# Optimization experiments

Hardware: AMD Instinct MI355X
Metric: run time of the kernel (lower is better)

The kernel has to match this reference:

```python
import jax, jax.numpy as jnp
import numpy as np

B, S, H, I, E_ROUTED, TOP_K = 8, 2048, 1024, 2048, 8, 2


def _expert(x, Wg, Wu, Wd):
    # SwiGLU expert: down(silu(gate(x)) * up(x)); Linear weights stored [out, in]
    return (jax.nn.silu(x @ Wg.T) * (x @ Wu.T)) @ Wd.T


def setup_inputs() -> dict:
    key = jax.random.key(0)
    ks = jax.random.split(key, 9)
    s = 0.02  # init scale
    return {
        "x": jax.random.normal(ks[0], (B, S, H), dtype=jnp.float32),
        # shared expert (num_shared = 1)
        "Wg_s": jax.random.normal(ks[1], (I, H), dtype=jnp.float32) * s,
        "Wu_s": jax.random.normal(ks[2], (I, H), dtype=jnp.float32) * s,
        "Wd_s": jax.random.normal(ks[3], (H, I), dtype=jnp.float32) * s,
        # routed experts, stacked [E, ...]
        "Wg": jax.random.normal(ks[4], (E_ROUTED, I, H), dtype=jnp.float32) * s,
        "Wu": jax.random.normal(ks[5], (E_ROUTED, I, H), dtype=jnp.float32) * s,
        "Wd": jax.random.normal(ks[6], (E_ROUTED, H, I), dtype=jnp.float32) * s,
        # router
        "Wr": jax.random.normal(ks[7], (E_ROUTED, H), dtype=jnp.float32) * s,
        "rb": jnp.zeros((E_ROUTED,), dtype=jnp.float32),
    }


def reference(x, Wg_s, Wu_s, Wd_s, Wg, Wu, Wd, Wr, rb):
    # shared experts (num_shared = 1, so mean == the single expert output)
    shared = _expert(x, Wg_s, Wu_s, Wd_s)  # [B,S,H]

    # sigmoid top-k routing
    logits = jnp.einsum('bsh,eh->bse', x, Wr) + rb        # [B,S,E]
    probs = jax.nn.sigmoid(logits)
    scores, idx = jax.lax.top_k(probs, TOP_K)             # [B,S,K]

    # dense combine weights: cw[b,s,e] = sum_k scores[b,s,k] * 1[idx[b,s,k]==e]
    cw = (jax.nn.one_hot(idx, E_ROUTED, dtype=x.dtype) * scores[..., None]).sum(-2)  # [B,S,E]

    out = shared
    for e in range(E_ROUTED):  # small fixed expert count
        out = out + cw[..., e:e + 1] * _expert(x, Wg[e], Wu[e], Wd[e])
    return out
```

## Files before the change

kernel.cpp:

```cpp
#include <hip/hip_runtime.h>

#define T_TOK 16384
#define HDIM  1024
#define IDIM  2048
#define NEXP  8
#define CNT_STRIDE 32
#define TOK_PER_BLK 32
#define MAX_RTILES 264

typedef __attribute__((ext_vector_type(8))) short bf16x8;
typedef __attribute__((ext_vector_type(4))) float f32x4;
typedef unsigned short u16;
typedef unsigned int u32;

typedef __attribute__((address_space(1))) const unsigned int gas_u32;
typedef __attribute__((address_space(3))) unsigned int las_u32;

__device__ __forceinline__ void gl16(const void* g, void* l) {
  __builtin_amdgcn_global_load_lds((gas_u32*)g, (las_u32*)l, 16, 0, 0);
}

__device__ __forceinline__ u16 f2bf(float f) {
  union { float f; u32 i; } v; v.f = f;
  u32 r = v.i + 0x7FFF + ((v.i >> 16) & 1);
  return (u16)(r >> 16);
}
__device__ __forceinline__ u32 pack2(float a, float b) {
  return (u32)f2bf(a) | ((u32)f2bf(b) << 16);
}

__global__ __launch_bounds__(256) void cvt_kernel(
    const float* __restrict__ s, u16* __restrict__ d, int n)
{
  int i = (blockIdx.x * 256 + threadIdx.x) * 4;
  if (i < n) {
    f32x4 v = *(const f32x4*)(s + i);
    uint2 o; o.x = pack2(v[0], v[1]); o.y = pack2(v[2], v[3]);
    *(uint2*)(d + i) = o;
  }
}

__global__ void init_counts(int* counts) {
  counts[threadIdx.x] = 0;
}

__global__ __launch_bounds__(256) void router_kernel(
    const float* __restrict__ x, const float* __restrict__ Wr,
    const float* __restrict__ rb, float* __restrict__ cw,
    int* __restrict__ counts, int* __restrict__ lists)
{
  __shared__ __align__(16) float sWr[NEXP * HDIM];
  __shared__ int pickE[2 * TOK_PER_BLK];
  __shared__ int pickT[2 * TOK_PER_BLK];

  const int tid = threadIdx.x;
  const int lane = tid & 63;
  const int wv = tid >> 6;

  for (int i = tid; i < NEXP * HDIM / 4; i += 256)
    ((f32x4*)sWr)[i] = ((const f32x4*)Wr)[i];

  float rbl[NEXP];
  #pragma unroll
  for (int e = 0; e < NEXP; ++e) rbl[e] = rb[e];

  __syncthreads();

  const int t_base = blockIdx.x * TOK_PER_BLK + wv * (TOK_PER_BLK / 4);
  for (int j = 0; j < TOK_PER_BLK / 4; ++j) {
    const int t = t_base + j;
    const float* xrow = x + (size_t)t * HDIM;
    f32x4 xv[4];
    #pragma unroll
    for (int c = 0; c < 4; ++c) xv[c] = *(const f32x4*)(xrow + c * 256 + lane * 4);

    double acc[NEXP];
    #pragma unroll
    for (int e = 0; e < NEXP; ++e) {
      const float* wr = sWr + e * HDIM;
      double a = 0.0;
      #pragma unroll
      for (int c = 0; c < 4; ++c) {
        f32x4 w4 = *(const f32x4*)(wr + c * 256 + lane * 4);
        a += (double)xv[c][0] * (double)w4[0];
        a += (double)xv[c][1] * (double)w4[1];
        a += (double)xv[c][2] * (double)w4[2];
        a += (double)xv[c][3] * (double)w4[3];
      }
      acc[e] = a;
    }
    #pragma unroll
    for (int e = 0; e < NEXP; ++e) {
      double a = acc[e];
      a += __shfl_xor(a, 1, 64);
      a += __shfl_xor(a, 2, 64);
      a += __shfl_xor(a, 4, 64);
      acc[e] = a;
    }
    double s0 = (lane & 1) ? acc[1] : acc[0];
    double s1 = (lane & 1) ? acc[3] : acc[2];
    double s2 = (lane & 1) ? acc[5] : acc[4];
    double s3 = (lane & 1) ? acc[7] : acc[6];
    double u0 = (lane & 2) ? s1 : s0;
    double u1 = (lane & 2) ? s3 : s2;
    double v  = (lane & 4) ? u1 : u0;
    v += __shfl_xor(v, 8, 64);
    v += __shfl_xor(v, 16, 64);
    v += __shfl_xor(v, 32, 64);
    double l[NEXP];
    #pragma unroll
    for (int e = 0; e < NEXP; ++e) l[e] = __shfl(v, e, 64) + (double)rbl[e];

    if (lane == 0) {
      int i1 = 0;
      #pragma unroll
      for (int e = 1; e < NEXP; ++e) if (l[e] > l[i1]) i1 = e;
      int i2 = -1;
      #pragma unroll
      for (int e = 0; e < NEXP; ++e) {
        if (e == i1) continue;
        if (i2 < 0 || l[e] > l[i2]) i2 = e;
      }
      float p1 = (float)(1.0 / (1.0 + exp(-l[i1])));
      float p2 = (float)(1.0 / (1.0 + exp(-l[i2])));
      cw[(size_t)t * NEXP + i1] = p1;
      cw[(size_t)t * NEXP + i2] = p2;
      int slot = (wv * (TOK_PER_BLK / 4) + j) * 2;
      pickE[slot] = i1; pickE[slot + 1] = i2;
      pickT[slot] = t;  pickT[slot + 1] = t;
    }
  }
  __syncthreads();

  const int myE = pickE[lane];
  const int myT = pickT[lane];
  #pragma unroll
  for (int ei = 0; ei < 2; ++ei) {
    int e = wv + ei * 4;
    unsigned long long b = __ballot(myE == e);
    int cnt = __popcll(b);
    int base = 0;
    if (lane == 0) base = atomicAdd(&counts[e * CNT_STRIDE], cnt);
    base = __shfl(base, 0, 64);
    if (myE == e)
      lists[(size_t)e * T_TOK + base + __popcll(b & ((1ull << lane) - 1))] = myT;
  }
}

__global__ void build_tiles(const int* __restrict__ counts,
                            int* __restrict__ td_e, int* __restrict__ td_r0,
                            int* __restrict__ ntiles)
{
  if (threadIdx.x == 0) {
    int n = 0;
    for (int e = 0; e < NEXP; ++e) {
      int c = counts[e * CNT_STRIDE];
      for (int r = 0; r < c; r += 128) { td_e[n] = e; td_r0[n] = r; ++n; }
    }
    *ntiles = n;
  }
}

template<int SRC>
__global__ __launch_bounds__(256, 2) void moe_gateup_k(
    const u16* __restrict__ xb, const float* __restrict__ xf,
    const u16* __restrict__ Wg_b, const u16* __restrict__ Wu_b,
    const float* __restrict__ Wg_f, const float* __restrict__ Wu_f,
    const int* __restrict__ list, const int* __restrict__ count_ptr,
    u16* __restrict__ hbuf, int c0)
{
  __shared__ __align__(16) u16 sA[128 * 32];
  __shared__ __align__(16) u16 sG[128 * 32];
  __shared__ __align__(16) u16 sU[128 * 32];

  const int cnt = count_ptr ? *count_ptr : T_TOK;
  const int remain = cnt - c0;
  const int m0 = blockIdx.y * 128;
  if (m0 >= remain) return;
  const int n0 = blockIdx.x * 128;

  const int tid = threadIdx.x, lane = tid & 63, w = tid >> 6;
  const int wm = w & 1, wn = w >> 1;
  const int quad = lane >> 4, l15 = lane & 15;

  const int srow0 = w * 32 + (lane >> 2);
  const int srow1 = srow0 + 16;
  const int kch = (lane & 3) * 8;
  const int ar = lane >> 3, ac = lane & 7;

  const u16 *pa0 = nullptr, *pa1 = nullptr, *pg0 = nullptr, *pg1 = nullptr,
            *pu0 = nullptr, *pu1 = nullptr;
  const float *fa[4], *fg[4], *fu[4];
  int frow[4];

  if (SRC == 0) {
    int gi0 = c0 + m0 + srow0, gi1 = c0 + m0 + srow1;
    int tok0 = (gi0 < cnt) ? (list ? list[gi0] : gi0) : 0;
    int tok1 = (gi1 < cnt) ? (list ? list[gi1] : gi1) : 0;
    pa0 = xb + (size_t)tok0 * HDIM + kch;
    pa1 = xb + (size_t)tok1 * HDIM + kch;
    pg0 = Wg_b + (size_t)(n0 + srow0) * HDIM + kch;
    pg1 = Wg_b + (size_t)(n0 + srow1) * HDIM + kch;
    pu0 = Wu_b + (size_t)(n0 + srow0) * HDIM + kch;
    pu1 = Wu_b + (size_t)(n0 + srow1) * HDIM + kch;
  } else {
    #pragma unroll
    for (int p = 0; p < 4; ++p) {
      int row = w * 32 + p * 8 + ar;
      frow[p] = row;
      int gi = c0 + m0 + row;
      int tok = (gi < cnt) ? (list ? list[gi] : gi) : 0;
      fa[p] = xf + (size_t)tok * HDIM + ac * 4;
      fg[p] = Wg_f + (size_t)(n0 + row) * HDIM + ac * 4;
      fu[p] = Wu_f + (size_t)(n0 + row) * HDIM + ac * 4;
    }
  }

  const u16* fA = sA + (wm * 64 + l15) * 32 + quad * 8;
  const u16* fG = sG + (wn * 64 + l15) * 32 + quad * 8;
  const u16* fU = sU + (wn * 64 + l15) * 32 + quad * 8;

  f32x4 accG[4][4] = {};
  f32x4 accU[4][4] = {};

  for (int kt = 0; kt < HDIM / 32; ++kt) {
    if (SRC == 0) {
      gl16(pa0 + kt * 32, sA + w * 1024);
      gl16(pa1 + kt * 32, sA + w * 1024 + 512);
      gl16(pg0 + kt * 32, sG + w * 1024);
      gl16(pg1 + kt * 32, sG + w * 1024 + 512);
      gl16(pu0 + kt * 32, sU + w * 1024);
      gl16(pu1 + kt * 32, sU + w * 1024 + 512);
    } else {
      #pragma unroll
      for (int p = 0; p < 4; ++p) {
        f32x4 va = *(const f32x4*)(fa[p] + kt * 32);
        f32x4 vg = *(const f32x4*)(fg[p] + kt * 32);
        f32x4 vu = *(const f32x4*)(fu[p] + kt * 32);
        uint2 oa; oa.x = pack2(va[0], va[1]); oa.y = pack2(va[2], va[3]);
        uint2 og; og.x = pack2(vg[0], vg[1]); og.y = pack2(vg[2], vg[3]);
        uint2 ou; ou.x = pack2(vu[0], vu[1]); ou.y = pack2(vu[2], vu[3]);
        *(uint2*)(sA + frow[p] * 32 + ac * 4) = oa;
        *(uint2*)(sG + frow[p] * 32 + ac * 4) = og;
        *(uint2*)(sU + frow[p] * 32 + ac * 4) = ou;
      }
    }
    __syncthreads();
    bf16x8 a[4];
    #pragma unroll
    for (int mt = 0; mt < 4; ++mt) a[mt] = *(const bf16x8*)(fA + mt * 16 * 32);
    #pragma unroll
    for (int nt = 0; nt < 4; ++nt) {
      bf16x8 bg = *(const bf16x8*)(fG + nt * 16 * 32);
      bf16x8 bu = *(const bf16x8*)(fU + nt * 16 * 32);
      #pragma unroll
      for (int mt = 0; mt < 4; ++mt) {
        accG[mt][nt] = __builtin_amdgcn_mfma_f32_16x16x32_bf16(a[mt], bg, accG[mt][nt], 0, 0, 0);
        accU[mt][nt] = __builtin_amdgcn_mfma_f32_16x16x32_bf16(a[mt], bu, accU[mt][nt], 0, 0, 0);
      }
    }
    __syncthreads();
  }

  #pragma unroll
  for (int mt = 0; mt < 4; ++mt) {
    #pragma unroll
    for (int i = 0; i < 4; ++i) {
      int row = m0 + wm * 64 + mt * 16 + quad * 4 + i;
      if (row < remain) {
        u16* orow = hbuf + (size_t)row * IDIM + n0 + wn * 64 + l15;
        #pragma unroll
        for (int nt = 0; nt < 4; ++nt) {
          float g = accG[mt][nt][i], u = accU[mt][nt][i];
          float h = (g / (1.f + __expf(-g))) * u;
          orow[nt * 16] = f2bf(h);
        }
      }
    }
  }
}

template<int SRC>
__global__ __launch_bounds__(256, 2) void moe_down_k(
    const u16* __restrict__ hbuf,
    const u16* __restrict__ Wd_b, const float* __restrict__ Wd_f,
    const int* __restrict__ list, const int* __restrict__ count_ptr,
    const float* __restrict__ cw, int expert, float* __restrict__ out, int c0)
{
  __shared__ __align__(16) u16 sA[128 * 32];
  __shared__ __align__(16) u16 sB[128 * 32];

  const int cnt = count_ptr ? *count_ptr : T_TOK;
  const int remain = cnt - c0;
  const int m0 = blockIdx.y * 128;
  if (m0 >= remain) return;
  const int n0 = blockIdx.x * 128;

  const int tid = threadIdx.x, lane = tid & 63, w = tid >> 6;
  const int wm = w & 1, wn = w >> 1;
  const int quad = lane >> 4, l15 = lane & 15;

  const int srow0 = w * 32 + (lane >> 2);
  const int srow1 = srow0 + 16;
  const int kch = (lane & 3) * 8;
  const int ar = lane >> 3, ac = lane & 7;

  const u16* pa0 = hbuf + (size_t)(m0 + srow0) * IDIM + kch;
  const u16* pa1 = hbuf + (size_t)(m0 + srow1) * IDIM + kch;
  const u16 *pb0 = nullptr, *pb1 = nullptr;
  const float* fb[4];
  int frow[4];
  if (SRC == 0) {
    pb0 = Wd_b + (size_t)(n0 + srow0) * IDIM + kch;
    pb1 = Wd_b + (size_t)(n0 + srow1) * IDIM + kch;
  } else {
    #pragma unroll
    for (int p = 0; p < 4; ++p) {
      int row = w * 32 + p * 8 + ar;
      frow[p] = row;
      fb[p] = Wd_f + (size_t)(n0 + row) * IDIM + ac * 4;
    }
  }

  const u16* fA = sA + (wm * 64 + l15) * 32 + quad * 8;
  const u16* fB = sB + (wn * 64 + l15) * 32 + quad * 8;

  f32x4 acc[4][4] = {};

  for (int kt = 0; kt < IDIM / 32; ++kt) {
    gl16(pa0 + kt * 32, sA + w * 1024);
    gl16(pa1 + kt * 32, sA + w * 1024 + 512);
    if (SRC == 0) {
      gl16(pb0 + kt * 32, sB + w * 1024);
      gl16(pb1 + kt * 32, sB + w * 1024 + 512);
    } else {
      #pragma unroll
      for (int p = 0; p < 4; ++p) {
        f32x4 v = *(const f32x4*)(fb[p] + kt * 32);
        uint2 o; o.x = pack2(v[0], v[1]); o.y = pack2(v[2], v[3]);
        *(uint2*)(sB + frow[p] * 32 + ac * 4) = o;
      }
    }
    __syncthreads();
    bf16x8 a[4];
    #pragma unroll
    for (int mt = 0; mt < 4; ++mt) a[mt] = *(const bf16x8*)(fA + mt * 16 * 32);
    #pragma unroll
    for (int nt = 0; nt < 4; ++nt) {
      bf16x8 b = *(const bf16x8*)(fB + nt * 16 * 32);
      #pragma unroll
      for (int mt = 0; mt < 4; ++mt)
        acc[mt][nt] = __builtin_amdgcn_mfma_f32_16x16x32_bf16(a[mt], b, acc[mt][nt], 0, 0, 0);
    }
    __syncthreads();
  }

  #pragma unroll
  for (int mt = 0; mt < 4; ++mt) {
    #pragma unroll
    for (int i = 0; i < 4; ++i) {
      int rl = m0 + wm * 64 + mt * 16 + quad * 4 + i;
      if (rl < remain) {
        int token = list ? list[c0 + rl] : (c0 + rl);
        float s = (expert >= 0) ? cw[(size_t)token * NEXP + expert] : 1.f;
        float* orow = out + (size_t)token * HDIM + n0 + wn * 64 + l15;
        #pragma unroll
        for (int nt = 0; nt < 4; ++nt) {
          float v = s * acc[mt][nt][i];
          if (expert >= 0) v += orow[nt * 16];
          orow[nt * 16] = v;
        }
      }
    }
  }
}

__global__ __launch_bounds__(256, 2) void moe_gateup_fused(
    const u16* __restrict__ xb,
    const u16* __restrict__ Wg_b, const u16* __restrict__ Wu_b,
    const int* __restrict__ lists, const int* __restrict__ counts,
    const int* __restrict__ td_e, const int* __restrict__ td_r0,
    const int* __restrict__ ntiles,
    u16* __restrict__ hbuf, int t0)
{
  __shared__ __align__(16) u16 sA[128 * 32];
  __shared__ __align__(16) u16 sG[128 * 32];
  __shared__ __align__(16) u16 sU[128 * 32];

  const int ty = t0 + blockIdx.y;
  if (ty >= *ntiles) return;
  const int e = td_e[ty];
  const int r0 = td_r0[ty];
  const int cnt = counts[e * CNT_STRIDE];
  const int* list = lists + (size_t)e * T_TOK;
  const size_t WSH = (size_t)IDIM * HDIM;
  const u16* Wg_e = Wg_b + (size_t)e * WSH;
  const u16* Wu_e = Wu_b + (size_t)e * WSH;
  const int n0 = blockIdx.x * 128;

  const int tid = threadIdx.x, lane = tid & 63, w = tid >> 6;
  const int wm = w & 1, wn = w >> 1;
  const int quad = lane >> 4, l15 = lane & 15;

  const int srow0 = w * 32 + (lane >> 2);
  const int srow1 = srow0 + 16;
  const int kch = (lane & 3) * 8;

  int gi0 = r0 + srow0, gi1 = r0 + srow1;
  int tok0 = (gi0 < cnt) ? list[gi0] : 0;
  int tok1 = (gi1 < cnt) ? list[gi1] : 0;
  const u16* pa0 = xb + (size_t)tok0 * HDIM + kch;
  const u16* pa1 = xb + (size_t)tok1 * HDIM + kch;
  const u16* pg0 = Wg_e + (size_t)(n0 + srow0) * HDIM + kch;
  const u16* pg1 = Wg_e + (size_t)(n0 + srow1) * HDIM + kch;
  const u16* pu0 = Wu_e + (size_t)(n0 + srow0) * HDIM + kch;
  const u16* pu1 = Wu_e + (size_t)(n0 + srow1) * HDIM + kch;

  const u16* fA = sA + (wm * 64 + l15) * 32 + quad * 8;
  const u16* fG = sG + (wn * 64 + l15) * 32 + quad * 8;
  const u16* fU = sU + (wn * 64 + l15) * 32 + quad * 8;

  f32x4 accG[4][4] = {};
  f32x4 accU[4][4] = {};

  for (int kt = 0; kt < HDIM / 32; ++kt) {
    gl16(pa0 + kt * 32, sA + w * 1024);
    gl16(pa1 + kt * 32, sA + w * 1024 + 512);
    gl16(pg0 + kt * 32, sG + w * 1024);
    gl16(pg1 + kt * 32, sG + w * 1024 + 512);
    gl16(pu0 + kt * 32, sU + w * 1024);
    gl16(pu1 + kt * 32, sU + w * 1024 + 512);
    __syncthreads();
    bf16x8 a[4];
    #pragma unroll
    for (int mt = 0; mt < 4; ++mt) a[mt] = *(const bf16x8*)(fA + mt * 16 * 32);
    #pragma unroll
    for (int nt = 0; nt < 4; ++nt) {
      bf16x8 bg = *(const bf16x8*)(fG + nt * 16 * 32);
      bf16x8 bu = *(const bf16x8*)(fU + nt * 16 * 32);
      #pragma unroll
      for (int mt = 0; mt < 4; ++mt) {
        accG[mt][nt] = __builtin_amdgcn_mfma_f32_16x16x32_bf16(a[mt], bg, accG[mt][nt], 0, 0, 0);
        accU[mt][nt] = __builtin_amdgcn_mfma_f32_16x16x32_bf16(a[mt], bu, accU[mt][nt], 0, 0, 0);
      }
    }
    __syncthreads();
  }

  #pragma unroll
  for (int mt = 0; mt < 4; ++mt) {
    #pragma unroll
    for (int i = 0; i < 4; ++i) {
      int rl = wm * 64 + mt * 16 + quad * 4 + i;
      u16* orow = hbuf + (size_t)(blockIdx.y * 128 + rl) * IDIM + n0 + wn * 64 + l15;
      #pragma unroll
      for (int nt = 0; nt < 4; ++nt) {
        float g = accG[mt][nt][i], u = accU[mt][nt][i];
        float h = (g / (1.f + __expf(-g))) * u;
        orow[nt * 16] = f2bf(h);
      }
    }
  }
}

__global__ __launch_bounds__(256, 2) void moe_down_fused(
    const u16* __restrict__ hbuf, const u16* __restrict__ Wd_b,
    const int* __restrict__ lists, const int* __restrict__ counts,
    const int* __restrict__ td_e, const int* __restrict__ td_r0,
    const int* __restrict__ ntiles,
    const float* __restrict__ cw, float* __restrict__ out, int t0)
{
  __shared__ __align__(16) u16 sA[128 * 32];
  __shared__ __align__(16) u16 sB[128 * 32];

  const int ty = t0 + blockIdx.y;
  if (ty >= *ntiles) return;
  const int e = td_e[ty];
  const int r0 = td_r0[ty];
  const int cnt = counts[e * CNT_STRIDE];
  const int* list = lists + (size_t)e * T_TOK;
  const size_t WSH = (size_t)IDIM * HDIM;
  const u16* Wd_e = Wd_b + (size_t)e * WSH;
  const int n0 = blockIdx.x * 128;

  const int tid = threadIdx.x, lane = tid & 63, w = tid >> 6;
  const int wm = w & 1, wn = w >> 1;
  const int quad = lane >> 4, l15 = lane & 15;

  const int srow0 = w * 32 + (lane >> 2);
  const int srow1 = srow0 + 16;
  const int kch = (lane & 3) * 8;

  const u16* pa0 = hbuf + (size_t)(blockIdx.y * 128 + srow0) * IDIM + kch;
  const u16* pa1 = hbuf + (size_t)(blockIdx.y * 128 + srow1) * IDIM + kch;
  const u16* pb0 = Wd_e + (size_t)(n0 + srow0) * IDIM + kch;
  const u16* pb1 = Wd_e + (size_t)(n0 + srow1) * IDIM + kch;

  const u16* fA = sA + (wm * 64 + l15) * 32 + quad * 8;
  const u16* fB = sB + (wn * 64 + l15) * 32 + quad * 8;

  f32x4 acc[4][4] = {};

  for (int kt = 0; kt < IDIM / 32; ++kt) {
    gl16(pa0 + kt * 32, sA + w * 1024);
    gl16(pa1 + kt * 32, sA + w * 1024 + 512);
    gl16(pb0 + kt * 32, sB + w * 1024);
    gl16(pb1 + kt * 32, sB + w * 1024 + 512);
    __syncthreads();
    bf16x8 a[4];
    #pragma unroll
    for (int mt = 0; mt < 4; ++mt) a[mt] = *(const bf16x8*)(fA + mt * 16 * 32);
    #pragma unroll
    for (int nt = 0; nt < 4; ++nt) {
      bf16x8 b = *(const bf16x8*)(fB + nt * 16 * 32);
      #pragma unroll
      for (int mt = 0; mt < 4; ++mt)
        acc[mt][nt] = __builtin_amdgcn_mfma_f32_16x16x32_bf16(a[mt], b, acc[mt][nt], 0, 0, 0);
    }
    __syncthreads();
  }

  #pragma unroll
  for (int mt = 0; mt < 4; ++mt) {
    #pragma unroll
    for (int i = 0; i < 4; ++i) {
      int rl = wm * 64 + mt * 16 + quad * 4 + i;
      if (r0 + rl < cnt) {
        int token = list[r0 + rl];
        float s = cw[(size_t)token * NEXP + e];
        float* orow = out + (size_t)token * HDIM + n0 + wn * 64 + l15;
        #pragma unroll
        for (int nt = 0; nt < 4; ++nt)
          atomicAdd(&orow[nt * 16], s * acc[mt][nt][i]);
      }
    }
  }
}

extern "C" void kernel_launch(void* const* d_in, const int* in_sizes, int n_in,
                              void* d_out, int out_size, void* d_ws, size_t ws_size,
                              hipStream_t stream) {
  (void)in_sizes; (void)n_in; (void)out_size;
  const float* x    = (const float*)d_in[0];
  const float* Wg_s = (const float*)d_in[1];
  const float* Wu_s = (const float*)d_in[2];
  const float* Wd_s = (const float*)d_in[3];
  const float* Wg   = (const float*)d_in[4];
  const float* Wu   = (const float*)d_in[5];
  const float* Wd   = (const float*)d_in[6];
  const float* Wr   = (const float*)d_in[7];
  const float* rb   = (const float*)d_in[8];
  float* out = (float*)d_out;

  char* ws = (char*)d_ws;
  size_t off = 1024;
  int* counts = (int*)ws;
  int* lists = (int*)(ws + off);  off += (size_t)NEXP * T_TOK * 4;
  float* cw = (float*)(ws + off); off += (size_t)T_TOK * NEXP * 4;
  int* td = (int*)(ws + off);     off += 2304;
  int* td_e = td;
  int* td_r0 = td + MAX_RTILES;
  int* ntiles = td + 2 * MAX_RTILES;

  const size_t WSH = (size_t)IDIM * HDIM;
  const size_t xc_elems = (size_t)T_TOK * HDIM;
  const size_t wc_elems = 3 * WSH + 3 * NEXP * WSH;
  const size_t fast_need = off + (xc_elems + wc_elems) * 2 + (size_t)2048 * IDIM * 2;
  const bool fast = ws_size >= fast_need;

  u16* xc = (u16*)(ws + off);
  u16* wgs_c = xc + (fast ? xc_elems : 0);
  u16* wus_c = wgs_c + WSH;
  u16* wds_c = wus_c + WSH;
  u16* wg_c = wds_c + WSH;
  u16* wu_c = wg_c + NEXP * WSH;
  u16* wd_c = wu_c + NEXP * WSH;

  size_t hoff = off + (fast ? (xc_elems + wc_elems) * 2 : 0);
  u16* hbuf = (u16*)(ws + hoff);

  size_t avail = (ws_size > hoff) ? (ws_size - hoff) : 0;
  long long capll = (long long)(avail / ((size_t)IDIM * 2));
  int cap = (capll > T_TOK) ? T_TOK : (int)capll;
  cap &= ~127;
  if (cap < 128) cap = 128;
  int nchunks = (T_TOK + cap - 1) / cap;

  init_counts<<<1, NEXP * CNT_STRIDE, 0, stream>>>(counts);
  if (fast) {
    auto cv = [&](const float* s, u16* d, size_t n) {
      int blocks = (int)((n / 4 + 255) / 256);
      cvt_kernel<<<blocks, 256, 0, stream>>>(s, d, (int)n);
    };
    cv(x, xc, xc_elems);
    cv(Wg_s, wgs_c, WSH); cv(Wu_s, wus_c, WSH); cv(Wd_s, wds_c, WSH);
    cv(Wg, wg_c, NEXP * WSH); cv(Wu, wu_c, NEXP * WSH); cv(Wd, wd_c, NEXP * WSH);
  }
  router_kernel<<<T_TOK / TOK_PER_BLK, 256, 0, stream>>>(x, Wr, rb, cw, counts, lists);

  dim3 blk(256);
  dim3 gA(IDIM / 128, cap / 128);
  dim3 gB(HDIM / 128, cap / 128);

  for (int c = 0; c < nchunks; ++c) {
    int c0 = c * cap;
    if (fast) {
      moe_gateup_k<0><<<gA, blk, 0, stream>>>(xc, nullptr, wgs_c, wus_c, nullptr, nullptr,
                                              nullptr, nullptr, hbuf, c0);
      moe_down_k<0><<<gB, blk, 0, stream>>>(hbuf, wds_c, nullptr, nullptr, nullptr,
                                            cw, -1, out, c0);
    } else {
      moe_gateup_k<1><<<gA, blk, 0, stream>>>(nullptr, x, nullptr, nullptr, Wg_s, Wu_s,
                                              nullptr, nullptr, hbuf, c0);
      moe_down_k<1><<<gB, blk, 0, stream>>>(hbuf, nullptr, Wd_s, nullptr, nullptr,
                                            cw, -1, out, c0);
    }
  }

  if (fast) {
    build_tiles<<<1, 64, 0, stream>>>(counts, td_e, td_r0, ntiles);
    int tpc = cap / 128;
    for (int t0 = 0; t0 < MAX_RTILES; t0 += tpc) {
      int ytiles = (MAX_RTILES - t0 < tpc) ? (MAX_RTILES - t0) : tpc;
      dim3 gAf(IDIM / 128, ytiles);
      dim3 gBf(HDIM / 128, ytiles);
      moe_gateup_fused<<<gAf, blk, 0, stream>>>(xc, wg_c, wu_c, lists, counts,
                                                td_e, td_r0, ntiles, hbuf, t0);
      moe_down_fused<<<gBf, blk, 0, stream>>>(hbuf, wd_c, lists, counts,
                                              td_e, td_r0, ntiles, cw, out, t0);
    }
  } else {
    for (int e = 0; e < NEXP; ++e) {
      const int* lst = lists + (size_t)e * T_TOK;
      const int* cptr = counts + (size_t)e * CNT_STRIDE;
      for (int c = 0; c < nchunks; ++c) {
        int c0 = c * cap;
        moe_gateup_k<1><<<gA, blk, 0, stream>>>(nullptr, x, nullptr, nullptr,
                                                Wg + (size_t)e * WSH, Wu + (size_t)e * WSH,
                                                lst, cptr, hbuf, c0);
        moe_down_k<1><<<gB, blk, 0, stream>>>(hbuf, nullptr, Wd + (size_t)e * WSH,
                                              lst, cptr, cw, e, out, c0);
      }
    }
  }
}
```

Baseline: 1.272 ms.

## Merge shared expert into routed tile list with BK=64 swizzled tiles and 256-wide down

Folds the shared expert into the same tile descriptor list as the routed experts (expert id -1), so one pair of grouped GEMM launches covers all work. Output is zeroed first and every contribution is accumulated with atomics. The kernels now use a K-tile of 64 with an XOR-swizzled LDS layout to avoid bank conflicts and halve the barrier count. The down projection uses a 128x256 tile to get more reuse per loaded A tile. The costs are more atomic traffic on the shared-expert output, a separate zeroing pass, and larger LDS use that may limit occupancy.

```diff
diff --git a/kernel.cpp b/kernel.cpp
--- a/kernel.cpp
+++ b/kernel.cpp
@@ -6,7 +6,7 @@
 #define NEXP  8
 #define CNT_STRIDE 32
 #define TOK_PER_BLK 32
-#define MAX_RTILES 264
+#define MAX_TILES 400
 
 typedef __attribute__((ext_vector_type(8))) short bf16x8;
 typedef __attribute__((ext_vector_type(4))) float f32x4;
@@ -42,6 +42,12 @@
 
 __global__ void init_counts(int* counts) {
   counts[threadIdx.x] = 0;
+}
+
+__global__ __launch_bounds__(256) void zero_kernel(float* __restrict__ p, int n4) {
+  f32x4 z = {0.f, 0.f, 0.f, 0.f};
+  for (int i = blockIdx.x * 256 + threadIdx.x; i < n4; i += gridDim.x * 256)
+    ((f32x4*)p)[i] = z;
 }
 
 __global__ __launch_bounds__(256) void router_kernel(
@@ -153,6 +159,7 @@
 {
   if (threadIdx.x == 0) {
     int n = 0;
+    for (int r = 0; r < T_TOK; r += 128) { td_e[n] = -1; td_r0[n] = r; ++n; }
     for (int e = 0; e < NEXP; ++e) {
       int c = counts[e * CNT_STRIDE];
       for (int r = 0; r < c; r += 128) { td_e[n] = e; td_r0[n] = r; ++n; }
@@ -161,10 +168,201 @@
   }
 }
 
-template<int SRC>
+
+__global__ __launch_bounds__(256, 2) void gateup128f(
+    const u16* __restrict__ xb,
+    const u16* __restrict__ Wg_sh, const u16* __restrict__ Wu_sh,
+    const u16* __restrict__ Wg_rt, const u16* __restrict__ Wu_rt,
+    const int* __restrict__ lists, const int* __restrict__ counts,
+    const int* __restrict__ td_e, const int* __restrict__ td_r0,
+    const int* __restrict__ ntiles,
+    u16* __restrict__ hbuf, int t0)
+{
+  __shared__ __align__(16) u16 sA[128 * 64];
+  __shared__ __align__(16) u16 sG[128 * 64];
+  __shared__ __align__(16) u16 sU[128 * 64];
+
+  const int ty = t0 + blockIdx.y;
+  if (ty >= *ntiles) return;
+  const int e = td_e[ty];
+  const int r0 = td_r0[ty];
+  const size_t WSH = (size_t)IDIM * HDIM;
+  int cnt; const int* list; const u16 *Wg_e, *Wu_e;
+  if (e < 0) { cnt = T_TOK; list = nullptr; Wg_e = Wg_sh; Wu_e = Wu_sh; }
+  else {
+    cnt = counts[e * CNT_STRIDE]; list = lists + (size_t)e * T_TOK;
+    Wg_e = Wg_rt + (size_t)e * WSH; Wu_e = Wu_rt + (size_t)e * WSH;
+  }
+  const int n0 = blockIdx.x * 128;
+
+  const int tid = threadIdx.x, lane = tid & 63, w = tid >> 6;
+  const int wm = w & 1, wn = w >> 1;
+  const int quad = lane >> 4, l15 = lane & 15, l7 = lane & 7;
+  const int drow = lane >> 3;
+  const int sslot = (lane & 7) ^ drow;
+
+  const u16 *pa[4], *pg[4], *pu[4];
+  u16 *dA[4], *dG[4], *dU[4];
+  #pragma unroll
+  for (int c = 0; c < 4; ++c) {
+    int row = w * 32 + c * 8 + drow;
+    int gi = r0 + row;
+    int tok = list ? ((gi < cnt) ? list[gi] : 0) : gi;
+    pa[c] = xb + (size_t)tok * HDIM + sslot * 8;
+    pg[c] = Wg_e + (size_t)(n0 + row) * HDIM + sslot * 8;
+    pu[c] = Wu_e + (size_t)(n0 + row) * HDIM + sslot * 8;
+    dA[c] = sA + (w * 32 + c * 8) * 64;
+    dG[c] = sG + (w * 32 + c * 8) * 64;
+    dU[c] = sU + (w * 32 + c * 8) * 64;
+  }
+
+  const u16* fA = sA + (wm * 64 + l15) * 64;
+  const u16* fG = sG + (wn * 64 + l15) * 64;
+  const u16* fU = sU + (wn * 64 + l15) * 64;
+
+  f32x4 accG[4][4] = {};
+  f32x4 accU[4][4] = {};
+
+  for (int kt = 0; kt < HDIM / 64; ++kt) {
+    #pragma unroll
+    for (int c = 0; c < 4; ++c) {
+      gl16(pa[c] + kt * 64, dA[c]);
+      gl16(pg[c] + kt * 64, dG[c]);
+      gl16(pu[c] + kt * 64, dU[c]);
+    }
+    __syncthreads();
+    #pragma unroll
+    for (int ks = 0; ks < 2; ++ks) {
+      const int sw = ((ks * 4 + quad) ^ l7) * 8;
+      bf16x8 a[4], bg[4], bu[4];
+      #pragma unroll
+      for (int mt = 0; mt < 4; ++mt) a[mt] = *(const bf16x8*)(fA + mt * 1024 + sw);
+      #pragma unroll
+      for (int nt = 0; nt < 4; ++nt) {
+        bg[nt] = *(const bf16x8*)(fG + nt * 1024 + sw);
+        bu[nt] = *(const bf16x8*)(fU + nt * 1024 + sw);
+      }
+      #pragma unroll
+      for (int nt = 0; nt < 4; ++nt) {
+        #pragma unroll
+        for (int mt = 0; mt < 4; ++mt) {
+          accG[mt][nt] = __builtin_amdgcn_mfma_f32_16x16x32_bf16(a[mt], bg[nt], accG[mt][nt], 0, 0, 0);
+          accU[mt][nt] = __builtin_amdgcn_mfma_f32_16x16x32_bf16(a[mt], bu[nt], accU[mt][nt], 0, 0, 0);
+        }
+      }
+    }
+    __syncthreads();
+  }
+
+  #pragma unroll
+  for (int mt = 0; mt < 4; ++mt) {
+    #pragma unroll
+    for (int i = 0; i < 4; ++i) {
+      int rl = wm * 64 + mt * 16 + quad * 4 + i;
+      u16* orow = hbuf + (size_t)(blockIdx.y * 128 + rl) * IDIM + n0 + wn * 64 + l15;
+      #pragma unroll
+      for (int nt = 0; nt < 4; ++nt) {
+        float g = accG[mt][nt][i], u = accU[mt][nt][i];
+        float h = (g / (1.f + __expf(-g))) * u;
+        orow[nt * 16] = f2bf(h);
+      }
+    }
+  }
+}
+
+__global__ __launch_bounds__(256, 2) void down256f(
+    const u16* __restrict__ hbuf,
+    const u16* __restrict__ Wd_sh, const u16* __restrict__ Wd_rt,
+    const int* __restrict__ lists, const int* __restrict__ counts,
+    const int* __restrict__ td_e, const int* __restrict__ td_r0,
+    const int* __restrict__ ntiles,
+    const float* __restrict__ cw, float* __restrict__ out, int t0)
+{
+  __shared__ __align__(16) u16 sA[128 * 64];
+  __shared__ __align__(16) u16 sB[256 * 64];
+
+  const int ty = t0 + blockIdx.y;
+  if (ty >= *ntiles) return;
+  const int e = td_e[ty];
+  const int r0 = td_r0[ty];
+  const size_t WSH = (size_t)IDIM * HDIM;
+  int cnt; const int* list; const u16* Wd_e;
+  if (e < 0) { cnt = T_TOK; list = nullptr; Wd_e = Wd_sh; }
+  else {
+    cnt = counts[e * CNT_STRIDE]; list = lists + (size_t)e * T_TOK;
+    Wd_e = Wd_rt + (size_t)e * WSH;
+  }
+  const int n0 = blockIdx.x * 256;
+
+  const int tid = threadIdx.x, lane = tid & 63, w = tid >> 6;
+  const int wm = w & 1, wn = w >> 1;
+  const int quad = lane >> 4, l15 = lane & 15, l7 = lane & 7;
+  const int drow = lane >> 3;
+  const int sslot = (lane & 7) ^ drow;
+
+  const u16 *pa[4], *pb[8];
+  u16 *dA[4], *dB[8];
+  #pragma unroll
+  for (int c = 0; c < 4; ++c) {
+    int row = w * 32 + c * 8 + drow;
+    pa[c] = hbuf + (size_t)(blockIdx.y * 128 + row) * IDIM + sslot * 8;
+    dA[c] = sA + (w * 32 + c * 8) * 64;
+  }
+  #pragma unroll
+  for (int c = 0; c < 8; ++c) {
+    int row = w * 64 + c * 8 + drow;
+    pb[c] = Wd_e + (size_t)(n0 + row) * IDIM + sslot * 8;
+    dB[c] = sB + (w * 64 + c * 8) * 64;
+  }
+
+  const u16* fA = sA + (wm * 64 + l15) * 64;
+  const u16* fB = sB + (wn * 128 + l15) * 64;
+
+  f32x4 acc[4][8] = {};
+
+  for (int kt = 0; kt < IDIM / 64; ++kt) {
+    #pragma unroll
+    for (int c = 0; c < 4; ++c) gl16(pa[c] + kt * 64, dA[c]);
+    #pragma unroll
+    for (int c = 0; c < 8; ++c) gl16(pb[c] + kt * 64, dB[c]);
+    __syncthreads();
+    #pragma unroll
+    for (int ks = 0; ks < 2; ++ks) {
+      const int sw = ((ks * 4 + quad) ^ l7) * 8;
+      bf16x8 a[4], b[8];
+      #pragma unroll
+      for (int mt = 0; mt < 4; ++mt) a[mt] = *(const bf16x8*)(fA + mt * 1024 + sw);
+      #pragma unroll
+      for (int nt = 0; nt < 8; ++nt) b[nt] = *(const bf16x8*)(fB + nt * 1024 + sw);
+      #pragma unroll
+      for (int nt = 0; nt < 8; ++nt) {
+        #pragma unroll
+        for (int mt = 0; mt < 4; ++mt)
+          acc[mt][nt] = __builtin_amdgcn_mfma_f32_16x16x32_bf16(a[mt], b[nt], acc[mt][nt], 0, 0, 0);
+      }
+    }
+    __syncthreads();
+  }
+
+  #pragma unroll
+  for (int mt = 0; mt < 4; ++mt) {
+    #pragma unroll
+    for (int i = 0; i < 4; ++i) {
+      int rl = wm * 64 + mt * 16 + quad * 4 + i;
+      if (r0 + rl < cnt) {
+        int token = list ? list[r0 + rl] : (r0 + rl);
+        float s = (e >= 0) ? cw[(size_t)token * NEXP + e] : 1.f;
+        float* orow = out + (size_t)token * HDIM + n0 + wn * 128 + l15;
+        #pragma unroll
+        for (int nt = 0; nt < 8; ++nt)
+          atomicAdd(&orow[nt * 16], s * acc[mt][nt][i]);
+      }
+    }
+  }
+}
+
 __global__ __launch_bounds__(256, 2) void moe_gateup_k(
-    const u16* __restrict__ xb, const float* __restrict__ xf,
-    const u16* __restrict__ Wg_b, const u16* __restrict__ Wu_b,
+    const float* __restrict__ xf,
     const float* __restrict__ Wg_f, const float* __restrict__ Wu_f,
     const int* __restrict__ list, const int* __restrict__ count_ptr,
     u16* __restrict__ hbuf, int c0)
@@ -182,38 +380,19 @@
   const int tid = threadIdx.x, lane = tid & 63, w = tid >> 6;
   const int wm = w & 1, wn = w >> 1;
   const int quad = lane >> 4, l15 = lane & 15;
-
-  const int srow0 = w * 32 + (lane >> 2);
-  const int srow1 = srow0 + 16;
-  const int kch = (lane & 3) * 8;
   const int ar = lane >> 3, ac = lane & 7;
 
-  const u16 *pa0 = nullptr, *pa1 = nullptr, *pg0 = nullptr, *pg1 = nullptr,
-            *pu0 = nullptr, *pu1 = nullptr;
   const float *fa[4], *fg[4], *fu[4];
   int frow[4];
-
-  if (SRC == 0) {
-    int gi0 = c0 + m0 + srow0, gi1 = c0 + m0 + srow1;
-    int tok0 = (gi0 < cnt) ? (list ? list[gi0] : gi0) : 0;
-    int tok1 = (gi1 < cnt) ? (list ? list[gi1] : gi1) : 0;
-    pa0 = xb + (size_t)tok0 * HDIM + kch;
-    pa1 = xb + (size_t)tok1 * HDIM + kch;
-    pg0 = Wg_b + (size_t)(n0 + srow0) * HDIM + kch;
-    pg1 = Wg_b + (size_t)(n0 + srow1) * HDIM + kch;
-    pu0 = Wu_b + (size_t)(n0 + srow0) * HDIM + kch;
-    pu1 = Wu_b + (size_t)(n0 + srow1) * HDIM + kch;
-  } else {
-    #pragma unroll
-    for (int p = 0; p < 4; ++p) {
-      int row = w * 32 + p * 8 + ar;
-      frow[p] = row;
-      int gi = c0 + m0 + row;
-      int tok = (gi < cnt) ? (list ? list[gi] : gi) : 0;
-      fa[p] = xf + (size_t)tok * HDIM + ac * 4;
-      fg[p] = Wg_f + (size_t)(n0 + row) * HDIM + ac * 4;
-      fu[p] = Wu_f + (size_t)(n0 + row) * HDIM + ac * 4;
-    }
+  #pragma unroll
+  for (int p = 0; p < 4; ++p) {
+    int row = w * 32 + p * 8 + ar;
+    frow[p] = row;
+    int gi = c0 + m0 + row;
+    int tok = (gi < cnt) ? (list ? list[gi] : gi) : 0;
+    fa[p] = xf + (size_t)tok * HDIM + ac * 4;
+    fg[p] = Wg_f + (size_t)(n0 + row) * HDIM + ac * 4;
+    fu[p] = Wu_f + (size_t)(n0 + row) * HDIM + ac * 4;
   }
 
   const u16* fA = sA + (wm * 64 + l15) * 32 + quad * 8;
@@ -224,26 +403,17 @@
   f32x4 accU[4][4] = {};
 
   for (int kt = 0; kt < HDIM / 32; ++kt) {
-    if (SRC == 0) {
-      gl16(pa0 + kt * 32, sA + w * 1024);
-      gl16(pa1 + kt * 32, sA + w * 1024 + 512);
-      gl16(pg0 + kt * 32, sG + w * 1024);
-      gl16(pg1 + kt * 32, sG + w * 1024 + 512);
-      gl16(pu0 + kt * 32, sU + w * 1024);
-      gl16(pu1 + kt * 32, sU + w * 1024 + 512);
-    } else {
-      #pragma unroll
-      for (int p = 0; p < 4; ++p) {
-        f32x4 va = *(const f32x4*)(fa[p] + kt * 32);
-        f32x4 vg = *(const f32x4*)(fg[p] + kt * 32);
-        f32x4 vu = *(const f32x4*)(fu[p] + kt * 32);
-        uint2 oa; oa.x = pack2(va[0], va[1]); oa.y = pack2(va[2], va[3]);
-        uint2 og; og.x = pack2(vg[0], vg[1]); og.y = pack2(vg[2], vg[3]);
-        uint2 ou; ou.x = pack2(vu[0], vu[1]); ou.y = pack2(vu[2], vu[3]);
-        *(uint2*)(sA + frow[p] * 32 + ac * 4) = oa;
-        *(uint2*)(sG + frow[p] * 32 + ac * 4) = og;
-        *(uint2*)(sU + frow[p] * 32 + ac * 4) = ou;
-      }
+    #pragma unroll
+    for (int p = 0; p < 4; ++p) {
+      f32x4 va = *(const f32x4*)(fa[p] + kt * 32);
+      f32x4 vg = *(const f32x4*)(fg[p] + kt * 32);
+      f32x4 vu = *(const f32x4*)(fu[p] + kt * 32);
+      uint2 oa; oa.x = pack2(va[0], va[1]); oa.y = pack2(va[2], va[3]);
+      uint2 og; og.x = pack2(vg[0], vg[1]); og.y = pack2(vg[2], vg[3]);
+      uint2 ou; ou.x = pack2(vu[0], vu[1]); ou.y = pack2(vu[2], vu[3]);
+      *(uint2*)(sA + frow[p] * 32 + ac * 4) = oa;
+      *(uint2*)(sG + frow[p] * 32 + ac * 4) = og;
+      *(uint2*)(sU + frow[p] * 32 + ac * 4) = ou;
     }
     __syncthreads();
     bf16x8 a[4];
@@ -280,10 +450,8 @@
   }
 }
 
-template<int SRC>
 __global__ __launch_bounds__(256, 2) void moe_down_k(
-    const u16* __restrict__ hbuf,
-    const u16* __restrict__ Wd_b, const float* __restrict__ Wd_f,
+    const u16* __restrict__ hbuf, const float* __restrict__ Wd_f,
     const int* __restrict__ list, const int* __restrict__ count_ptr,
     const float* __restrict__ cw, int expert, float* __restrict__ out, int c0)
 {
@@ -307,19 +475,13 @@
 
   const u16* pa0 = hbuf + (size_t)(m0 + srow0) * IDIM + kch;
   const u16* pa1 = hbuf + (size_t)(m0 + srow1) * IDIM + kch;
-  const u16 *pb0 = nullptr, *pb1 = nullptr;
   const float* fb[4];
   int frow[4];
-  if (SRC == 0) {
-    pb0 = Wd_b + (size_t)(n0 + srow0) * IDIM + kch;
-    pb1 = Wd_b + (size_t)(n0 + srow1) * IDIM + kch;
-  } else {
-    #pragma unroll
-    for (int p = 0; p < 4; ++p) {
-      int row = w * 32 + p * 8 + ar;
-      frow[p] = row;
-      fb[p] = Wd_f + (size_t)(n0 + row) * IDIM + ac * 4;
-    }
+  #pragma unroll
+  for (int p = 0; p < 4; ++p) {
+    int row = w * 32 + p * 8 + ar;
+    frow[p] = row;
+    fb[p] = Wd_f + (size_t)(n0 + row) * IDIM + ac * 4;
   }
 
   const u16* fA = sA + (wm * 64 + l15) * 32 + quad * 8;
@@ -330,16 +492,11 @@
   for (int kt = 0; kt < IDIM / 32; ++kt) {
     gl16(pa0 + kt * 32, sA + w * 1024);
     gl16(pa1 + kt * 32, sA + w * 1024 + 512);
-    if (SRC == 0) {
-      gl16(pb0 + kt * 32, sB + w * 1024);
-      gl16(pb1 + kt * 32, sB + w * 1024 + 512);
-    } else {
-      #pragma unroll
-      for (int p = 0; p < 4; ++p) {
-        f32x4 v = *(const f32x4*)(fb[p] + kt * 32);
-        uint2 o; o.x = pack2(v[0], v[1]); o.y = pack2(v[2], v[3]);
-        *(uint2*)(sB + frow[p] * 32 + ac * 4) = o;
-      }
+    #pragma unroll
+    for (int p = 0; p < 4; ++p) {
+      f32x4 v = *(const f32x4*)(fb[p] + kt * 32);
+      uint2 o; o.x = pack2(v[0], v[1]); o.y = pack2(v[2], v[3]);
+      *(uint2*)(sB + frow[p] * 32 + ac * 4) = o;
     }
     __syncthreads();
     bf16x8 a[4];
@@ -370,168 +527,6 @@
           if (expert >= 0) v += orow[nt * 16];
           orow[nt * 16] = v;
         }
-      }
-    }
-  }
-}
-
-__global__ __launch_bounds__(256, 2) void moe_gateup_fused(
-    const u16* __restrict__ xb,
-    const u16* __restrict__ Wg_b, const u16* __restrict__ Wu_b,
-    const int* __restrict__ lists, const int* __restrict__ counts,
-    const int* __restrict__ td_e, const int* __restrict__ td_r0,
-    const int* __restrict__ ntiles,
-    u16* __restrict__ hbuf, int t0)
-{
-  __shared__ __align__(16) u16 sA[128 * 32];
-  __shared__ __align__(16) u16 sG[128 * 32];
-  __shared__ __align__(16) u16 sU[128 * 32];
-
-  const int ty = t0 + blockIdx.y;
-  if (ty >= *ntiles) return;
-  const int e = td_e[ty];
-  const int r0 = td_r0[ty];
-  const int cnt = counts[e * CNT_STRIDE];
-  const int* list = lists + (size_t)e * T_TOK;
-  const size_t WSH = (size_t)IDIM * HDIM;
-  const u16* Wg_e = Wg_b + (size_t)e * WSH;
-  const u16* Wu_e = Wu_b + (size_t)e * WSH;
-  const int n0 = blockIdx.x * 128;
-
-  const int tid = threadIdx.x, lane = tid & 63, w = tid >> 6;
-  const int wm = w & 1, wn = w >> 1;
-  const int quad = lane >> 4, l15 = lane & 15;
-
-  const int srow0 = w * 32 + (lane >> 2);
-  const int srow1 = srow0 + 16;
-  const int kch = (lane & 3) * 8;
-
-  int gi0 = r0 + srow0, gi1 = r0 + srow1;
-  int tok0 = (gi0 < cnt) ? list[gi0] : 0;
-  int tok1 = (gi1 < cnt) ? list[gi1] : 0;
-  const u16* pa0 = xb + (size_t)tok0 * HDIM + kch;
-  const u16* pa1 = xb + (size_t)tok1 * HDIM + kch;
-  const u16* pg0 = Wg_e + (size_t)(n0 + srow0) * HDIM + kch;
-  const u16* pg1 = Wg_e + (size_t)(n0 + srow1) * HDIM + kch;
-  const u16* pu0 = Wu_e + (size_t)(n0 + srow0) * HDIM + kch;
-  const u16* pu1 = Wu_e + (size_t)(n0 + srow1) * HDIM + kch;
-
-  const u16* fA = sA + (wm * 64 + l15) * 32 + quad * 8;
-  const u16* fG = sG + (wn * 64 + l15) * 32 + quad * 8;
-  const u16* fU = sU + (wn * 64 + l15) * 32 + quad * 8;
-
-  f32x4 accG[4][4] = {};
-  f32x4 accU[4][4] = {};
-
-  for (int kt = 0; kt < HDIM / 32; ++kt) {
-    gl16(pa0 + kt * 32, sA + w * 1024);
-    gl16(pa1 + kt * 32, sA + w * 1024 + 512);
-    gl16(pg0 + kt * 32, sG + w * 1024);
-    gl16(pg1 + kt * 32, sG + w * 1024 + 512);
-    gl16(pu0 + kt * 32, sU + w * 1024);
-    gl16(pu1 + kt * 32, sU + w * 1024 + 512);
-    __syncthreads();
-    bf16x8 a[4];
-    #pragma unroll
-    for (int mt = 0; mt < 4; ++mt) a[mt] = *(const bf16x8*)(fA + mt * 16 * 32);
-    #pragma unroll
-    for (int nt = 0; nt < 4; ++nt) {
-      bf16x8 bg = *(const bf16x8*)(fG + nt * 16 * 32);
-      bf16x8 bu = *(const bf16x8*)(fU + nt * 16 * 32);
-      #pragma unroll
-      for (int mt = 0; mt < 4; ++mt) {
-        accG[mt][nt] = __builtin_amdgcn_mfma_f32_16x16x32_bf16(a[mt], bg, accG[mt][nt], 0, 0, 0);
-        accU[mt][nt] = __builtin_amdgcn_mfma_f32_16x16x32_bf16(a[mt], bu, accU[mt][nt], 0, 0, 0);
-      }
-    }
-    __syncthreads();
-  }
-
-  #pragma unroll
-  for (int mt = 0; mt < 4; ++mt) {
-    #pragma unroll
-    for (int i = 0; i < 4; ++i) {
-      int rl = wm * 64 + mt * 16 + quad * 4 + i;
-      u16* orow = hbuf + (size_t)(blockIdx.y * 128 + rl) * IDIM + n0 + wn * 64 + l15;
-      #pragma unroll
-      for (int nt = 0; nt < 4; ++nt) {
-        float g = accG[mt][nt][i], u = accU[mt][nt][i];
-        float h = (g / (1.f + __expf(-g))) * u;
-        orow[nt * 16] = f2bf(h);
-      }
-    }
-  }
-}
-
-__global__ __launch_bounds__(256, 2) void moe_down_fused(
-    const u16* __restrict__ hbuf, const u16* __restrict__ Wd_b,
-    const int* __restrict__ lists, const int* __restrict__ counts,
-    const int* __restrict__ td_e, const int* __restrict__ td_r0,
-    const int* __restrict__ ntiles,
-    const float* __restrict__ cw, float* __restrict__ out, int t0)
-{
-  __shared__ __align__(16) u16 sA[128 * 32];
-  __shared__ __align__(16) u16 sB[128 * 32];
-
-  const int ty = t0 + blockIdx.y;
-  if (ty >= *ntiles) return;
-  const int e = td_e[ty];
-  const int r0 = td_r0[ty];
-  const int cnt = counts[e * CNT_STRIDE];
-  const int* list = lists + (size_t)e * T_TOK;
-  const size_t WSH = (size_t)IDIM * HDIM;
-  const u16* Wd_e = Wd_b + (size_t)e * WSH;
-  const int n0 = blockIdx.x * 128;
-
-  const int tid = threadIdx.x, lane = tid & 63, w = tid >> 6;
-  const int wm = w & 1, wn = w >> 1;
-  const int quad = lane >> 4, l15 = lane & 15;
-
-  const int srow0 = w * 32 + (lane >> 2);
-  const int srow1 = srow0 + 16;
-  const int kch = (lane & 3) * 8;
-
-  const u16* pa0 = hbuf + (size_t)(blockIdx.y * 128 + srow0) * IDIM + kch;
-  const u16* pa1 = hbuf + (size_t)(blockIdx.y * 128 + srow1) * IDIM + kch;
-  const u16* pb0 = Wd_e + (size_t)(n0 + srow0) * IDIM + kch;
-  const u16* pb1 = Wd_e + (size_t)(n0 + srow1) * IDIM + kch;
-
-  const u16* fA = sA + (wm * 64 + l15) * 32 + quad * 8;
-  const u16* fB = sB + (wn * 64 + l15) * 32 + quad * 8;
-
-  f32x4 acc[4][4] = {};
-
-  for (int kt = 0; kt < IDIM / 32; ++kt) {
-    gl16(pa0 + kt * 32, sA + w * 1024);
-    gl16(pa1 + kt * 32, sA + w * 1024 + 512);
-    gl16(pb0 + kt * 32, sB + w * 1024);
-    gl16(pb1 + kt * 32, sB + w * 1024 + 512);
-    __syncthreads();
-    bf16x8 a[4];
-    #pragma unroll
-    for (int mt = 0; mt < 4; ++mt) a[mt] = *(const bf16x8*)(fA + mt * 16 * 32);
-    #pragma unroll
-    for (int nt = 0; nt < 4; ++nt) {
-      bf16x8 b = *(const bf16x8*)(fB + nt * 16 * 32);
-      #pragma unroll
-      for (int mt = 0; mt < 4; ++mt)
-        acc[mt][nt] = __builtin_amdgcn_mfma_f32_16x16x32_bf16(a[mt], b, acc[mt][nt], 0, 0, 0);
-    }
-    __syncthreads();
-  }
-
-  #pragma unroll
-  for (int mt = 0; mt < 4; ++mt) {
-    #pragma unroll
-    for (int i = 0; i < 4; ++i) {
-      int rl = wm * 64 + mt * 16 + quad * 4 + i;
-      if (r0 + rl < cnt) {
-        int token = list[r0 + rl];
-        float s = cw[(size_t)token * NEXP + e];
-        float* orow = out + (size_t)token * HDIM + n0 + wn * 64 + l15;
-        #pragma unroll
-        for (int nt = 0; nt < 4; ++nt)
-          atomicAdd(&orow[nt * 16], s * acc[mt][nt][i]);
       }
     }
   }
@@ -557,10 +552,10 @@
   int* counts = (int*)ws;
   int* lists = (int*)(ws + off);  off += (size_t)NEXP * T_TOK * 4;
   float* cw = (float*)(ws + off); off += (size_t)T_TOK * NEXP * 4;
-  int* td = (int*)(ws + off);     off += 2304;
+  int* td = (int*)(ws + off);     off += 3328;
   int* td_e = td;
-  int* td_r0 = td + MAX_RTILES;
-  int* ntiles = td + 2 * MAX_RTILES;
+  int* td_r0 = td + MAX_TILES;
+  int* ntiles = td + 2 * MAX_TILES;
 
   const size_t WSH = (size_t)IDIM * HDIM;
   const size_t xc_elems = (size_t)T_TOK * HDIM;
@@ -581,13 +576,13 @@
 
   size_t avail = (ws_size > hoff) ? (ws_size - hoff) : 0;
   long long capll = (long long)(avail / ((size_t)IDIM * 2));
-  int cap = (capll > T_TOK) ? T_TOK : (int)capll;
+  int cap = (capll > (long long)MAX_TILES * 128) ? MAX_TILES * 128 : (int)capll;
   cap &= ~127;
   if (cap < 128) cap = 128;
-  int nchunks = (T_TOK + cap - 1) / cap;
 
   init_counts<<<1, NEXP * CNT_STRIDE, 0, stream>>>(counts);
   if (fast) {
+    zero_kernel<<<2048, 256, 0, stream>>>(out, (int)(xc_elems / 4));
     auto cv = [&](const float* s, u16* d, size_t n) {
       int blocks = (int)((n / 4 + 255) / 256);
       cvt_kernel<<<blocks, 256, 0, stream>>>(s, d, (int)n);
@@ -598,49 +593,37 @@
   }
   router_kernel<<<T_TOK / TOK_PER_BLK, 256, 0, stream>>>(x, Wr, rb, cw, counts, lists);
 
-  dim3 blk(256);
-  dim3 gA(IDIM / 128, cap / 128);
-  dim3 gB(HDIM / 128, cap / 128);
-
-  for (int c = 0; c < nchunks; ++c) {
-    int c0 = c * cap;
-    if (fast) {
-      moe_gateup_k<0><<<gA, blk, 0, stream>>>(xc, nullptr, wgs_c, wus_c, nullptr, nullptr,
-                                              nullptr, nullptr, hbuf, c0);
-      moe_down_k<0><<<gB, blk, 0, stream>>>(hbuf, wds_c, nullptr, nullptr, nullptr,
-                                            cw, -1, out, c0);
-    } else {
-      moe_gateup_k<1><<<gA, blk, 0, stream>>>(nullptr, x, nullptr, nullptr, Wg_s, Wu_s,
-                                              nullptr, nullptr, hbuf, c0);
-      moe_down_k<1><<<gB, blk, 0, stream>>>(hbuf, nullptr, Wd_s, nullptr, nullptr,
-                                            cw, -1, out, c0);
-    }
-  }
-
   if (fast) {
     build_tiles<<<1, 64, 0, stream>>>(counts, td_e, td_r0, ntiles);
     int tpc = cap / 128;
-    for (int t0 = 0; t0 < MAX_RTILES; t0 += tpc) {
-      int ytiles = (MAX_RTILES - t0 < tpc) ? (MAX_RTILES - t0) : tpc;
-      dim3 gAf(IDIM / 128, ytiles);
-      dim3 gBf(HDIM / 128, ytiles);
-      moe_gateup_fused<<<gAf, blk, 0, stream>>>(xc, wg_c, wu_c, lists, counts,
-                                                td_e, td_r0, ntiles, hbuf, t0);
-      moe_down_fused<<<gBf, blk, 0, stream>>>(hbuf, wd_c, lists, counts,
-                                              td_e, td_r0, ntiles, cw, out, t0);
+    for (int t0 = 0; t0 < MAX_TILES; t0 += tpc) {
+      int yt = (MAX_TILES - t0 < tpc) ? (MAX_TILES - t0) : tpc;
+      gateup128f<<<dim3(IDIM / 128, yt), 256, 0, stream>>>(
+          xc, wgs_c, wus_c, wg_c, wu_c, lists, counts, td_e, td_r0, ntiles, hbuf, t0);
+      down256f<<<dim3(HDIM / 256, yt), 256, 0, stream>>>(
+          hbuf, wds_c, wd_c, lists, counts, td_e, td_r0, ntiles, cw, out, t0);
     }
   } else {
+    int fcap = cap;
+    int nchunks = (T_TOK + fcap - 1) / fcap;
+    dim3 blk(256);
+    dim3 gA(IDIM / 128, fcap / 128);
+    dim3 gB(HDIM / 128, fcap / 128);
+    for (int c = 0; c < nchunks; ++c) {
+      int c0 = c * fcap;
+      moe_gateup_k<<<gA, blk, 0, stream>>>(x, Wg_s, Wu_s, nullptr, nullptr, hbuf, c0);
+      moe_down_k<<<gB, blk, 0, stream>>>(hbuf, Wd_s, nullptr, nullptr, cw, -1, out, c0);
+    }
     for (int e = 0; e < NEXP; ++e) {
       const int* lst = lists + (size_t)e * T_TOK;
       const int* cptr = counts + (size_t)e * CNT_STRIDE;
       for (int c = 0; c < nchunks; ++c) {
-        int c0 = c * cap;
-        moe_gateup_k<1><<<gA, blk, 0, stream>>>(nullptr, x, nullptr, nullptr,
-                                                Wg + (size_t)e * WSH, Wu + (size_t)e * WSH,
-                                                lst, cptr, hbuf, c0);
-        moe_down_k<1><<<gB, blk, 0, stream>>>(hbuf, nullptr, Wd + (size_t)e * WSH,
-                                              lst, cptr, cw, e, out, c0);
-      }
-    }
-  }
-}
+        int c0 = c * fcap;
+        moe_gateup_k<<<gA, blk, 0, stream>>>(x, Wg + (size_t)e * WSH, Wu + (size_t)e * WSH,
+                                             lst, cptr, hbuf, c0);
+        moe_down_k<<<gB, blk, 0, stream>>>(hbuf, Wd + (size_t)e * WSH,
+                                           lst, cptr, cw, e, out, c0);
+      }
+    }
+  }
+}
```

Result: faster. 1.216 ms (-4.4%).
